# Optimization experiments

Measured on AMD Instinct MI355X. Metric: run time of the kernel, lower is better.

The kernel has to match this reference:

```python
import jax, jax.numpy as jnp
import numpy as np

N = 100000
C = 20
D = 2001
REG = 0.001


def setup_inputs() -> dict:
    key = jax.random.key(0)
    k1, k2, k3, k4 = jax.random.split(key, 4)
    weights = jax.random.normal(k1, (C, D), dtype=jnp.float32)
    X = jax.random.normal(k2, (N, D), dtype=jnp.float32)
    Y = jax.random.randint(k3, (N,), 0, C, dtype=jnp.int64)
    init_weights = jax.random.uniform(k4, (C, D), dtype=jnp.float32)
    return {"weights": weights, "X": X, "Y": Y, "init_weights": init_weights}


def reference(weights, X, Y, init_weights):
    # scores[i, c] = X[i] . weights[c]  -> one batched GEMM [N,D]x[D,C]
    scores = jnp.einsum('nd,cd->nc', X, weights)
    # matmul(weights[Y[i]], X[i]) = scores[i, Y[i]]
    picked = jnp.take_along_axis(scores, Y[:, None].astype(jnp.int32), axis=1)[:, 0]  # [N]
    # logsumexp over classes of -X[i].weights (stable, single pass)
    lse = jax.nn.logsumexp(-scores, axis=1)  # [N]
    data_loss = jnp.mean(picked + lse)
    # torch.norm(self.weights, 2) on a matrix = Frobenius norm of init_weights (constant wrt input weights)
    reg = REG * jnp.sqrt(jnp.sum(init_weights * init_weights))
    return data_loss + reg
```

## Files before the change

### kernel.cpp

```cpp
#include <hip/hip_runtime.h>
#include <math.h>

#define DD 2001
#define CC 20
#define NN 100000
#define REGC 0.001f

#define NSLICE 4
#define NRG 1563

#define PART_BYTES ((size_t)NSLICE * CC * NN * 4)

__device__ __forceinline__ float4 ld4(const float* p) {
  return *reinterpret_cast<const float4*>(p);
}

__global__ __launch_bounds__(64, 4) void loss_partial(
    const float* __restrict__ X,
    const float* __restrict__ Wt,
    float* __restrict__ part) {
  __shared__ float xs[64 * 20];
  __shared__ float wc[16 * 20];
  const int lane = threadIdx.x;
  const int rg = blockIdx.x;
  const int slice = blockIdx.y;
  const int rowbase = rg * 64;
  const int row0 = rowbase + lane;
  const bool valid = row0 < NN;

  const int ch0 = (slice == 0) ? 0 : (32 + 31 * (slice - 1));
  const int nch = (slice == 0) ? 32 : 31;

  const int srow = lane >> 2;
  const int sf = lane & 3;
  unsigned sb[4];
#pragma unroll
  for (int q = 0; q < 4; ++q) {
    int r = rowbase + q * 16 + srow;
    r = r < NN ? r : NN - 1;
    sb[q] = (unsigned)r * DD + sf * 4u;
  }

  float acc[CC];
#pragma unroll
  for (int c = 0; c < CC; ++c) acc[c] = 0.f;

  float4 xa[4];
  float4 wa0, wa1;
  {
    const unsigned doff = (unsigned)ch0 * 16u;
#pragma unroll
    for (int q = 0; q < 4; ++q) xa[q] = ld4(X + sb[q] + doff);
    const float* wp = Wt + (size_t)ch0 * (16 * CC);
    wa0 = ld4(wp + lane * 4);
    wa1 = (lane < 16) ? ld4(wp + 256 + lane * 4)
                      : float4{0, 0, 0, 0};
  }

#pragma unroll 1
  for (int ch = 0; ch < nch; ++ch) {
#pragma unroll
    for (int q = 0; q < 4; ++q)
      *reinterpret_cast<float4*>(&xs[(q * 16 + srow) * 20 + sf * 4]) = xa[q];
    *reinterpret_cast<float4*>(&wc[lane * 4]) = wa0;
    if (lane < 16) *reinterpret_cast<float4*>(&wc[256 + lane * 4]) = wa1;

    if (ch + 1 < nch) {
      const unsigned doff = (unsigned)(ch0 + ch + 1) * 16u;
#pragma unroll
      for (int q = 0; q < 4; ++q) xa[q] = ld4(X + sb[q] + doff);
      const float* wp = Wt + (size_t)(ch0 + ch + 1) * (16 * CC);
      wa0 = ld4(wp + lane * 4);
      if (lane < 16) wa1 = ld4(wp + 256 + lane * 4);
    }

#pragma unroll
    for (int f = 0; f < 4; ++f) {
      const float4 xv = *reinterpret_cast<const float4*>(&xs[lane * 20 + f * 4]);
      const float xj[4] = {xv.x, xv.y, xv.z, xv.w};
#pragma unroll
      for (int j = 0; j < 4; ++j) {
        const int d = f * 4 + j;
        const float xx = xj[j];
        const float4 w0 = *reinterpret_cast<const float4*>(&wc[d * 20 + 0]);
        const float4 w1 = *reinterpret_cast<const float4*>(&wc[d * 20 + 4]);
        const float4 w2 = *reinterpret_cast<const float4*>(&wc[d * 20 + 8]);
        const float4 w3 = *reinterpret_cast<const float4*>(&wc[d * 20 + 12]);
        const float4 w4 = *reinterpret_cast<const float4*>(&wc[d * 20 + 16]);
        acc[0] = fmaf(xx, w0.x, acc[0]);   acc[1] = fmaf(xx, w0.y, acc[1]);
        acc[2] = fmaf(xx, w0.z, acc[2]);   acc[3] = fmaf(xx, w0.w, acc[3]);
        acc[4] = fmaf(xx, w1.x, acc[4]);   acc[5] = fmaf(xx, w1.y, acc[5]);
        acc[6] = fmaf(xx, w1.z, acc[6]);   acc[7] = fmaf(xx, w1.w, acc[7]);
        acc[8] = fmaf(xx, w2.x, acc[8]);   acc[9] = fmaf(xx, w2.y, acc[9]);
        acc[10] = fmaf(xx, w2.z, acc[10]); acc[11] = fmaf(xx, w2.w, acc[11]);
        acc[12] = fmaf(xx, w3.x, acc[12]); acc[13] = fmaf(xx, w3.y, acc[13]);
        acc[14] = fmaf(xx, w3.z, acc[14]); acc[15] = fmaf(xx, w3.w, acc[15]);
        acc[16] = fmaf(xx, w4.x, acc[16]); acc[17] = fmaf(xx, w4.y, acc[17]);
        acc[18] = fmaf(xx, w4.z, acc[18]); acc[19] = fmaf(xx, w4.w, acc[19]);
      }
    }
  }

  if (slice == NSLICE - 1) {
    const int r = valid ? row0 : NN - 1;
    const float xx = X[(size_t)r * DD + 2000];
#pragma unroll
    for (int c = 0; c < CC; ++c)
      acc[c] = fmaf(xx, Wt[2000 * CC + c], acc[c]);
  }

  if (valid) {
    float* pb = part + (size_t)slice * CC * NN + row0;
#pragma unroll
    for (int c = 0; c < CC; ++c) pb[(size_t)c * NN] = acc[c];
  }
}

__global__ __launch_bounds__(256) void loss_epilogue(
    const float* __restrict__ part,
    const int* __restrict__ Y,
    float* __restrict__ out) {
  const int i = blockIdx.x * 256 + threadIdx.x;
  const bool valid = i < NN;
  const int row = valid ? i : NN - 1;

  float sc[CC];
#pragma unroll
  for (int c = 0; c < CC; ++c) {
    float s = 0.f;
#pragma unroll
    for (int sl = 0; sl < NSLICE; ++sl)
      s += part[((size_t)(sl * CC + c)) * NN + row];
    sc[c] = s;
  }

  float mx = -3.402823466e38f;
#pragma unroll
  for (int c = 0; c < CC; ++c) mx = fmaxf(mx, -sc[c]);
  float se = 0.f;
#pragma unroll
  for (int c = 0; c < CC; ++c) se += __expf(-sc[c] - mx);
  const int y = valid ? Y[row] : 0;
  float picked = 0.f;
#pragma unroll
  for (int c = 0; c < CC; ++c) picked = (c == y) ? sc[c] : picked;
  float li = valid ? (picked + mx + __logf(se)) : 0.f;

#pragma unroll
  for (int off = 32; off > 0; off >>= 1) li += __shfl_xor(li, off, 64);
  __shared__ float red[4];
  if ((threadIdx.x & 63) == 0) red[threadIdx.x >> 6] = li;
  __syncthreads();
  if (threadIdx.x == 0)
    atomicAdd(out, (red[0] + red[1] + red[2] + red[3]) * (1.0f / NN));
}

__global__ void reg_kernel(const float* __restrict__ IW, float* __restrict__ out) {
  __shared__ float red[256];
  float s = 0.f;
  for (int i = threadIdx.x; i < CC * DD; i += 256) {
    float v = IW[i];
    s += v * v;
  }
  red[threadIdx.x] = s;
  __syncthreads();
  for (int w = 128; w > 0; w >>= 1) {
    if (threadIdx.x < w) red[threadIdx.x] += red[threadIdx.x + w];
    __syncthreads();
  }
  if (threadIdx.x == 0) out[0] = REGC * sqrtf(red[0]);
}

__global__ void transpose_w(const float* __restrict__ W, float* __restrict__ Wt) {
  int i = blockIdx.x * 256 + threadIdx.x;
  if (i < CC * DD) {
    int c = i / DD;
    int d = i - c * DD;
    Wt[d * CC + c] = W[i];
  }
}

extern "C" void kernel_launch(void* const* d_in, const int* in_sizes, int n_in,
                              void* d_out, int out_size, void* d_ws, size_t ws_size,
                              hipStream_t stream) {
  const float* W  = (const float*)d_in[0];
  const float* X  = (const float*)d_in[1];
  const int*   Y  = (const int*)d_in[2];
  const float* IW = (const float*)d_in[3];
  float* out = (float*)d_out;

  float* part = (float*)d_ws;
  float* Wt = (float*)((char*)d_ws + PART_BYTES);

  reg_kernel<<<1, 256, 0, stream>>>(IW, out);
  transpose_w<<<(CC * DD + 255) / 256, 256, 0, stream>>>(W, Wt);
  dim3 grid(NRG, NSLICE);
  loss_partial<<<grid, 64, 0, stream>>>(X, Wt, part);
  loss_epilogue<<<(NN + 255) / 256, 256, 0, stream>>>(part, Y, out);
}
```

Measured before the change: 1.144 ms.

## Fuse K-slice partial sums and logsumexp epilogue into one block-level kernel

The four K-slices that were separate grid blocks become four wavefronts of one 256-thread block. Their partial class scores are reduced through shared memory, and the logsumexp loss epilogue runs in the same kernel. This removes the global partial-score buffer round trip (about 32 MB written and then read) and the epilogue launch. The regularizer and weight-transpose kernels are also merged into one prep launch. In exchange, each block holds more shared memory and needs a block barrier, and there are more atomics on the output (one per 64 rows).

New measurement: 1.139 ms. Within noise of the previous version (-0.4%).

```diff
diff --git a/kernel.cpp b/kernel.cpp
--- a/kernel.cpp
+++ b/kernel.cpp
@@ -6,30 +6,28 @@
 #define NN 100000
 #define REGC 0.001f
 
-#define NSLICE 4
 #define NRG 1563
-
-#define PART_BYTES ((size_t)NSLICE * CC * NN * 4)
 
 __device__ __forceinline__ float4 ld4(const float* p) {
   return *reinterpret_cast<const float4*>(p);
 }
 
-__global__ __launch_bounds__(64, 4) void loss_partial(
+__global__ __launch_bounds__(256, 4) void loss_fused(
     const float* __restrict__ X,
     const float* __restrict__ Wt,
-    float* __restrict__ part) {
-  __shared__ float xs[64 * 20];
-  __shared__ float wc[16 * 20];
-  const int lane = threadIdx.x;
-  const int rg = blockIdx.x;
-  const int slice = blockIdx.y;
-  const int rowbase = rg * 64;
+    const int* __restrict__ Y,
+    float* __restrict__ out) {
+  __shared__ float xs[4][64 * 20];
+  __shared__ float wc[4][16 * 20];
+  const int tid = threadIdx.x;
+  const int lane = tid & 63;
+  const int wid = tid >> 6;
+  const int rowbase = blockIdx.x * 64;
   const int row0 = rowbase + lane;
   const bool valid = row0 < NN;
 
-  const int ch0 = (slice == 0) ? 0 : (32 + 31 * (slice - 1));
-  const int nch = (slice == 0) ? 32 : 31;
+  const int ch0 = (wid == 0) ? 0 : (32 + 31 * (wid - 1));
+  const int nch = (wid == 0) ? 32 : 31;
 
   const int srow = lane >> 2;
   const int sf = lane & 3;
@@ -61,9 +59,9 @@
   for (int ch = 0; ch < nch; ++ch) {
 #pragma unroll
     for (int q = 0; q < 4; ++q)
-      *reinterpret_cast<float4*>(&xs[(q * 16 + srow) * 20 + sf * 4]) = xa[q];
-    *reinterpret_cast<float4*>(&wc[lane * 4]) = wa0;
-    if (lane < 16) *reinterpret_cast<float4*>(&wc[256 + lane * 4]) = wa1;
+      *reinterpret_cast<float4*>(&xs[wid][(q * 16 + srow) * 20 + sf * 4]) = xa[q];
+    *reinterpret_cast<float4*>(&wc[wid][lane * 4]) = wa0;
+    if (lane < 16) *reinterpret_cast<float4*>(&wc[wid][256 + lane * 4]) = wa1;
 
     if (ch + 1 < nch) {
       const unsigned doff = (unsigned)(ch0 + ch + 1) * 16u;
@@ -76,17 +74,17 @@
 
 #pragma unroll
     for (int f = 0; f < 4; ++f) {
-      const float4 xv = *reinterpret_cast<const float4*>(&xs[lane * 20 + f * 4]);
+      const float4 xv = *reinterpret_cast<const float4*>(&xs[wid][lane * 20 + f * 4]);
       const float xj[4] = {xv.x, xv.y, xv.z, xv.w};
 #pragma unroll
       for (int j = 0; j < 4; ++j) {
         const int d = f * 4 + j;
         const float xx = xj[j];
-        const float4 w0 = *reinterpret_cast<const float4*>(&wc[d * 20 + 0]);
-        const float4 w1 = *reinterpret_cast<const float4*>(&wc[d * 20 + 4]);
-        const float4 w2 = *reinterpret_cast<const float4*>(&wc[d * 20 + 8]);
-        const float4 w3 = *reinterpret_cast<const float4*>(&wc[d * 20 + 12]);
-        const float4 w4 = *reinterpret_cast<const float4*>(&wc[d * 20 + 16]);
+        const float4 w0 = *reinterpret_cast<const float4*>(&wc[wid][d * 20 + 0]);
+        const float4 w1 = *reinterpret_cast<const float4*>(&wc[wid][d * 20 + 4]);
+        const float4 w2 = *reinterpret_cast<const float4*>(&wc[wid][d * 20 + 8]);
+        const float4 w3 = *reinterpret_cast<const float4*>(&wc[wid][d * 20 + 12]);
+        const float4 w4 = *reinterpret_cast<const float4*>(&wc[wid][d * 20 + 16]);
         acc[0] = fmaf(xx, w0.x, acc[0]);   acc[1] = fmaf(xx, w0.y, acc[1]);
         acc[2] = fmaf(xx, w0.z, acc[2]);   acc[3] = fmaf(xx, w0.w, acc[3]);
         acc[4] = fmaf(xx, w1.x, acc[4]);   acc[5] = fmaf(xx, w1.y, acc[5]);
@@ -101,7 +99,7 @@
     }
   }
 
-  if (slice == NSLICE - 1) {
+  if (wid == 3) {
     const int r = valid ? row0 : NN - 1;
     const float xx = X[(size_t)r * DD + 2000];
 #pragma unroll
@@ -109,74 +107,70 @@
       acc[c] = fmaf(xx, Wt[2000 * CC + c], acc[c]);
   }
 
-  if (valid) {
-    float* pb = part + (size_t)slice * CC * NN + row0;
+  float* pl = &xs[0][0];
+  {
+    const int base = (wid * 64 + lane) * CC;
 #pragma unroll
-    for (int c = 0; c < CC; ++c) pb[(size_t)c * NN] = acc[c];
+    for (int f = 0; f < 5; ++f) {
+      float4 v = {acc[f * 4 + 0], acc[f * 4 + 1], acc[f * 4 + 2], acc[f * 4 + 3]};
+      *reinterpret_cast<float4*>(&pl[base + f * 4]) = v;
+    }
+  }
+  __syncthreads();
+
+  if (tid < 64) {
+    float sc[CC];
+#pragma unroll
+    for (int c = 0; c < CC; ++c) {
+      float s = 0.f;
+#pragma unroll
+      for (int w = 0; w < 4; ++w) s += pl[(w * 64 + lane) * CC + c];
+      sc[c] = s;
+    }
+
+    float mx = -3.402823466e38f;
+#pragma unroll
+    for (int c = 0; c < CC; ++c) mx = fmaxf(mx, -sc[c]);
+    float se = 0.f;
+#pragma unroll
+    for (int c = 0; c < CC; ++c) se += __expf(-sc[c] - mx);
+    const int y = valid ? Y[row0] : 0;
+    float picked = 0.f;
+#pragma unroll
+    for (int c = 0; c < CC; ++c) picked = (c == y) ? sc[c] : picked;
+    float li = valid ? (picked + mx + __logf(se)) : 0.f;
+
+#pragma unroll
+    for (int off = 32; off > 0; off >>= 1) li += __shfl_xor(li, off, 64);
+    if (tid == 0) atomicAdd(out, li * (1.0f / NN));
   }
 }
 
-__global__ __launch_bounds__(256) void loss_epilogue(
-    const float* __restrict__ part,
-    const int* __restrict__ Y,
+__global__ __launch_bounds__(256) void prep(
+    const float* __restrict__ W,
+    const float* __restrict__ IW,
+    float* __restrict__ Wt,
     float* __restrict__ out) {
   const int i = blockIdx.x * 256 + threadIdx.x;
-  const bool valid = i < NN;
-  const int row = valid ? i : NN - 1;
-
-  float sc[CC];
-#pragma unroll
-  for (int c = 0; c < CC; ++c) {
+  if (i < CC * DD) {
+    const int c = i / DD;
+    const int d = i - c * DD;
+    Wt[d * CC + c] = W[i];
+  }
+  if (blockIdx.x == 0) {
+    __shared__ float red[256];
     float s = 0.f;
-#pragma unroll
-    for (int sl = 0; sl < NSLICE; ++sl)
-      s += part[((size_t)(sl * CC + c)) * NN + row];
-    sc[c] = s;
-  }
-
-  float mx = -3.402823466e38f;
-#pragma unroll
-  for (int c = 0; c < CC; ++c) mx = fmaxf(mx, -sc[c]);
-  float se = 0.f;
-#pragma unroll
-  for (int c = 0; c < CC; ++c) se += __expf(-sc[c] - mx);
-  const int y = valid ? Y[row] : 0;
-  float picked = 0.f;
-#pragma unroll
-  for (int c = 0; c < CC; ++c) picked = (c == y) ? sc[c] : picked;
-  float li = valid ? (picked + mx + __logf(se)) : 0.f;
-
-#pragma unroll
-  for (int off = 32; off > 0; off >>= 1) li += __shfl_xor(li, off, 64);
-  __shared__ float red[4];
-  if ((threadIdx.x & 63) == 0) red[threadIdx.x >> 6] = li;
-  __syncthreads();
-  if (threadIdx.x == 0)
-    atomicAdd(out, (red[0] + red[1] + red[2] + red[3]) * (1.0f / NN));
-}
-
-__global__ void reg_kernel(const float* __restrict__ IW, float* __restrict__ out) {
-  __shared__ float red[256];
-  float s = 0.f;
-  for (int i = threadIdx.x; i < CC * DD; i += 256) {
-    float v = IW[i];
-    s += v * v;
-  }
-  red[threadIdx.x] = s;
-  __syncthreads();
-  for (int w = 128; w > 0; w >>= 1) {
-    if (threadIdx.x < w) red[threadIdx.x] += red[threadIdx.x + w];
+    for (int j = threadIdx.x; j < CC * DD; j += 256) {
+      const float v = IW[j];
+      s += v * v;
+    }
+    red[threadIdx.x] = s;
     __syncthreads();
-  }
-  if (threadIdx.x == 0) out[0] = REGC * sqrtf(red[0]);
-}
-
-__global__ void transpose_w(const float* __restrict__ W, float* __restrict__ Wt) {
-  int i = blockIdx.x * 256 + threadIdx.x;
-  if (i < CC * DD) {
-    int c = i / DD;
-    int d = i - c * DD;
-    Wt[d * CC + c] = W[i];
+    for (int w = 128; w > 0; w >>= 1) {
+      if (threadIdx.x < w) red[threadIdx.x] += red[threadIdx.x + w];
+      __syncthreads();
+    }
+    if (threadIdx.x == 0) out[0] = REGC * sqrtf(red[0]);
   }
 }
 
@@ -189,12 +183,8 @@
   const float* IW = (const float*)d_in[3];
   float* out = (float*)d_out;
 
-  float* part = (float*)d_ws;
-  float* Wt = (float*)((char*)d_ws + PART_BYTES);
+  float* Wt = (float*)d_ws;
 
-  reg_kernel<<<1, 256, 0, stream>>>(IW, out);
-  transpose_w<<<(CC * DD + 255) / 256, 256, 0, stream>>>(W, Wt);
-  dim3 grid(NRG, NSLICE);
-  loss_partial<<<grid, 64, 0, stream>>>(X, Wt, part);
-  loss_epilogue<<<(NN + 255) / 256, 256, 0, stream>>>(part, Y, out);
+  prep<<<(CC * DD + 255) / 256, 256, 0, stream>>>(W, IW, Wt, out);
+  loss_fused<<<NRG, 256, 0, stream>>>(X, Wt, Y, out);
 }
```
